# Kernel optimization log

Hardware: AMD Instinct MI355X
Metric: run time of the kernel (lower is better)

The kernel has to match this reference:

```python
import jax, jax.numpy as jnp
import numpy as np

T, B, XD, H, F = 1024, 256, 64, 256, 256  # seq_len, batch, x_dim, dim_RNN, feature dims
ALPHAS = [0.001, 0.01, 0.1]


def _alphas_per_unit():
    a = np.sort(np.asarray(ALPHAS, dtype=np.float32))
    assign = np.array([a[i % len(a)] for i in range(H)], dtype=np.float32)
    return jnp.asarray(np.sort(assign))  # [H]


def setup_inputs() -> dict:
    key = jax.random.key(0)
    ks = jax.random.split(key, 16)

    def w(k, shape, fan_in):
        return jax.random.normal(k, shape, jnp.float32) / np.sqrt(fan_in).astype(np.float32)

    return {
        "x": jax.random.normal(ks[0], (T, B, XD), jnp.float32),
        # feature_extractor_x: Linear(XD->F), Linear(F->F), tanh after each
        "Wx0": w(ks[1], (F, XD), XD), "bx0": jnp.zeros((F,), jnp.float32),
        "Wx1": w(ks[2], (F, F), F),   "bx1": jnp.zeros((F,), jnp.float32),
        # nn.RNN(F, H): tanh cell
        "Wih": w(ks[3], (H, F), F), "Whh": w(ks[4], (H, H), H),
        "bih": jnp.zeros((H,), jnp.float32), "bhh": jnp.zeros((H,), jnp.float32),
        # mlp_h_x: Linear(H->F), Linear(F->F), tanh after each
        "Wh0": w(ks[5], (F, H), H), "bh0": jnp.zeros((F,), jnp.float32),
        "Wh1": w(ks[6], (F, F), F), "bh1": jnp.zeros((F,), jnp.float32),
        # gen_out: Linear(F->XD)
        "Wg": w(ks[7], (XD, F), F), "bg": jnp.zeros((XD,), jnp.float32),
    }


def reference(x, Wx0, bx0, Wx1, bx1, Wih, Whh, bih, bhh, Wh0, bh0, Wh1, bh1, Wg, bg):
    act = jnp.tanh
    alphas = _alphas_per_unit()  # [H]

    # feature extractor applied to all timesteps at once (non-autonomous path)
    feat = act(jnp.einsum('tbx,fx->tbf', x, Wx0) + bx0)
    feat = act(jnp.einsum('tbf,gf->tbg', feat, Wx1) + bx1)  # [T,B,F]

    def step(h, ft):
        # y_t is generated from h BEFORE the recurrence update
        d = act(h @ Wh0.T + bh0)
        d = act(d @ Wh1.T + bh1)
        y = d @ Wg.T + bg  # [B,XD]
        h_raw = jnp.tanh(ft @ Wih.T + bih + h @ Whh.T + bhh)
        h_new = (1.0 - alphas) * h + alphas * h_raw  # leaky alpha-blend
        return h_new, y

    h0 = jnp.zeros((B, H), x.dtype)
    _, y = jax.lax.scan(step, h0, feat)  # y: [T,B,XD]
    return y
```

## Files before the change

### kernel.cpp

```cpp
#include <hip/hip_runtime.h>
#include <cstddef>


typedef _Float16 halfx8 __attribute__((ext_vector_type(8)));
typedef _Float16 halfx4 __attribute__((ext_vector_type(4)));
typedef float    f32x4  __attribute__((ext_vector_type(4)));

#define T_LEN 1024
#define B_SZ  256
#define H_DIM 256
#define M_ROWS (T_LEN * B_SZ)
#define MT     (M_ROWS / 32)
#define NRB    16
#define NGB    240

__device__ _Float16 gWx0[256 * 64];
__device__ _Float16 gWx1[256 * 256];
__device__ _Float16 gWih[256 * 256];
__device__ _Float16 gWh0[256 * 256];
__device__ _Float16 gWh1[256 * 256];
__device__ _Float16 gWg[64 * 256];
__device__ float gBx0[256], gBx1[256], gBih[256], gBh0[256], gBh1[256], gBg[64];
__device__ unsigned gProg[NRB];

__device__ __forceinline__ float fast_tanh(float x) {
  float e = __expf(2.0f * x);
  return 1.0f - 2.0f / (e + 1.0f);
}

__device__ __forceinline__ float alpha_of(int j) {
  return (j < 86) ? 0.001f : ((j < 171) ? 0.01f : 0.1f);
}

__device__ __forceinline__ void lds_barrier() {
  asm volatile("s_waitcnt lgkmcnt(0)\n\ts_barrier" ::: "memory");
}

__global__ void prep(const float* __restrict__ Wx0, const float* __restrict__ Wx1,
                     const float* __restrict__ Wih, const float* __restrict__ Wh0,
                     const float* __restrict__ Wh1, const float* __restrict__ Wg,
                     const float* __restrict__ bx0, const float* __restrict__ bx1,
                     const float* __restrict__ bih, const float* __restrict__ bh0,
                     const float* __restrict__ bh1, const float* __restrict__ bg) {
  const int i = blockIdx.x * blockDim.x + threadIdx.x;
  if (i < NRB) gProg[i] = 0u;
  if (i < 16384) { gWx0[i] = (_Float16)Wx0[i]; gWg[i] = (_Float16)Wg[i]; }
  if (i < 65536) {
    gWx1[i] = (_Float16)Wx1[i];
    gWih[i] = (_Float16)Wih[i];
    gWh0[i] = (_Float16)Wh0[i];
    gWh1[i] = (_Float16)Wh1[i];
  }
  if (i < 256) {
    gBx0[i] = bx0[i]; gBx1[i] = bx1[i]; gBih[i] = bih[i];
    gBh0[i] = bh0[i]; gBh1[i] = bh1[i];
  }
  if (i < 64) gBg[i] = bg[i];
}

template <int KCH, bool TANH>
__device__ __forceinline__ void stage_tile(const _Float16 (*__restrict__ Ah)[264],
                                           _Float16 (*__restrict__ Ch)[264],
                                           const _Float16* __restrict__ W,
                                           const float* __restrict__ bias,
                                           const int tid) {
  constexpr int K = KCH * 32;
  const int lane = tid & 63, wave = tid >> 6, l15 = lane & 15, quad = lane >> 4;
  const int jw = wave * 32;

  halfx8 Bf[2][KCH];
  float bcol[2];
  int jj[2];
#pragma unroll
  for (int nt = 0; nt < 2; nt++) {
    jj[nt] = jw + nt * 16 + l15;
    bcol[nt] = bias[jj[nt]];
#pragma unroll
    for (int ks = 0; ks < KCH; ks++)
      Bf[nt][ks] = *(const halfx8*)(W + (size_t)jj[nt] * K + ks * 32 + quad * 8);
  }

  f32x4 acc[2][2];
#pragma unroll
  for (int mi = 0; mi < 2; mi++)
#pragma unroll
    for (int nt = 0; nt < 2; nt++) acc[mi][nt] = (f32x4){0.f, 0.f, 0.f, 0.f};

#pragma unroll
  for (int ks = 0; ks < KCH; ks++)
#pragma unroll
    for (int mi = 0; mi < 2; mi++) {
      halfx8 a = *(const halfx8*)&Ah[mi * 16 + l15][ks * 32 + quad * 8];
#pragma unroll
      for (int nt = 0; nt < 2; nt++)
        acc[mi][nt] = __builtin_amdgcn_mfma_f32_16x16x32_f16(a, Bf[nt][ks], acc[mi][nt], 0, 0, 0);
    }

#pragma unroll
  for (int mi = 0; mi < 2; mi++)
#pragma unroll
    for (int nt = 0; nt < 2; nt++)
#pragma unroll
      for (int rg = 0; rg < 4; rg++) {
        float v = acc[mi][nt][rg] + bcol[nt];
        if (TANH) v = fast_tanh(v);
        Ch[mi * 16 + quad * 4 + rg][jj[nt]] = (_Float16)v;
      }
}

__device__ __forceinline__ void stage_zx(const _Float16 (*__restrict__ Ah)[264],
                                         _Float16* __restrict__ C,
                                         const _Float16* __restrict__ W,
                                         const float* __restrict__ bias,
                                         const int tid) {
  constexpr int KCH = 8, K = 256;
  const int lane = tid & 63, wave = tid >> 6, l15 = lane & 15, quad = lane >> 4;
  const int jw = wave * 32;

  halfx8 Bf[2][KCH];
  float bcol[2];
  int jj[2];
#pragma unroll
  for (int nt = 0; nt < 2; nt++) {
    jj[nt] = jw + nt * 16 + l15;
    bcol[nt] = bias[jj[nt]];
#pragma unroll
    for (int ks = 0; ks < KCH; ks++)
      Bf[nt][ks] = *(const halfx8*)(W + (size_t)jj[nt] * K + ks * 32 + quad * 8);
  }

  f32x4 acc[2][2];
#pragma unroll
  for (int mi = 0; mi < 2; mi++)
#pragma unroll
    for (int nt = 0; nt < 2; nt++) acc[mi][nt] = (f32x4){0.f, 0.f, 0.f, 0.f};

#pragma unroll
  for (int ks = 0; ks < KCH; ks++)
#pragma unroll
    for (int mi = 0; mi < 2; mi++) {
      halfx8 a = *(const halfx8*)&Ah[mi * 16 + l15][ks * 32 + quad * 8];
#pragma unroll
      for (int nt = 0; nt < 2; nt++)
        acc[mi][nt] = __builtin_amdgcn_mfma_f32_16x16x32_f16(a, Bf[nt][ks], acc[mi][nt], 0, 0, 0);
    }

#pragma unroll
  for (int mi = 0; mi < 2; mi++)
#pragma unroll
    for (int nt = 0; nt < 2; nt++)
#pragma unroll
      for (int rg = 0; rg < 4; rg++) {
        const int row = mi * 16 + quad * 4 + rg;
        C[(size_t)row * 256 + jj[nt]] = (_Float16)(acc[mi][nt][rg] + bcol[nt]);
      }
}

__device__ __forceinline__ void stage_out(const _Float16 (*__restrict__ Ah)[264],
                                          float* __restrict__ C,
                                          const _Float16* __restrict__ W,
                                          const float* __restrict__ bias,
                                          const int tid) {
  const int lane = tid & 63, wave = tid >> 6, l15 = lane & 15, quad = lane >> 4;
  if (wave < 4) {
    const int jcol = wave * 16 + l15;
    halfx8 Bf[8];
#pragma unroll
    for (int ks = 0; ks < 8; ks++)
      Bf[ks] = *(const halfx8*)(W + (size_t)jcol * 256 + ks * 32 + quad * 8);
    const float bc = bias[jcol];
    f32x4 acc[2];
#pragma unroll
    for (int mi = 0; mi < 2; mi++) acc[mi] = (f32x4){0.f, 0.f, 0.f, 0.f};
#pragma unroll
    for (int ks = 0; ks < 8; ks++)
#pragma unroll
      for (int mi = 0; mi < 2; mi++) {
        halfx8 a = *(const halfx8*)&Ah[mi * 16 + l15][ks * 32 + quad * 8];
        acc[mi] = __builtin_amdgcn_mfma_f32_16x16x32_f16(a, Bf[ks], acc[mi], 0, 0, 0);
      }
#pragma unroll
    for (int mi = 0; mi < 2; mi++)
#pragma unroll
      for (int rg = 0; rg < 4; rg++)
        C[(size_t)(mi * 16 + quad * 4 + rg) * 64 + jcol] = acc[mi][rg] + bc;
  }
}

__global__ __launch_bounds__(512, 2)
void pre(const float* __restrict__ x, _Float16* __restrict__ zx) {
  __shared__ __attribute__((aligned(16))) _Float16 lds[2][32][264];
  const int tid = threadIdx.x;
  _Float16(*Ah)[264] = lds[0];
  _Float16(*Bh)[264] = lds[1];

  for (int bm = blockIdx.x; bm < MT; bm += gridDim.x) {
    {
      const int srow = tid >> 4, sk4 = tid & 15;
      float4 tv = *(const float4*)(x + (size_t)(bm * 32 + srow) * 64 + sk4 * 4);
      halfx4 h;
      h[0] = (_Float16)tv.x; h[1] = (_Float16)tv.y;
      h[2] = (_Float16)tv.z; h[3] = (_Float16)tv.w;
      *(halfx4*)&Ah[srow][sk4 * 4] = h;
    }
    lds_barrier();
    stage_tile<2, true>(Ah, Bh, gWx0, gBx0, tid);
    lds_barrier();
    stage_tile<8, true>(Bh, Ah, gWx1, gBx1, tid);
    lds_barrier();
    stage_zx(Ah, zx + (size_t)bm * 32 * 256, gWih, gBih, tid);
    lds_barrier();
  }
}

__device__ void rnn_block(const _Float16* __restrict__ zx,
                          _Float16* __restrict__ h_all,
                          const float* __restrict__ Whh,
                          const float* __restrict__ bhh_p,
                          _Float16 (*__restrict__ lds)[264],
                          const int bid) {
  _Float16(*hB)[16][264] = reinterpret_cast<_Float16(*)[16][264]>(&lds[0][0]);

  const int tid  = threadIdx.x;
  const int lane = tid & 63;
  const int wave = tid >> 6;
  const int l15  = lane & 15;
  const int quad = lane >> 4;
  const int r0   = bid * 16;
  const int jb   = wave * 32;

  halfx8 Af[2][8];
#pragma unroll
  for (int mt = 0; mt < 2; mt++) {
    const int j = jb + mt * 16 + l15;
#pragma unroll
    for (int ks = 0; ks < 8; ks++) {
      const float* wp = Whh + (size_t)j * H_DIM + ks * 32 + quad * 8;
      float4 w0 = *(const float4*)wp;
      float4 w1 = *(const float4*)(wp + 4);
      halfx8 f;
      f[0] = (_Float16)w0.x; f[1] = (_Float16)w0.y;
      f[2] = (_Float16)w0.z; f[3] = (_Float16)w0.w;
      f[4] = (_Float16)w1.x; f[5] = (_Float16)w1.y;
      f[6] = (_Float16)w1.z; f[7] = (_Float16)w1.w;
      Af[mt][ks] = f;
    }
  }

  float bj[2][4], aj[2][4], oma[2][4];
#pragma unroll
  for (int mt = 0; mt < 2; mt++)
#pragma unroll
    for (int rg = 0; rg < 4; rg++) {
      const int j = jb + mt * 16 + quad * 4 + rg;
      bj[mt][rg]  = bhh_p[j];
      aj[mt][rg]  = alpha_of(j);
      oma[mt][rg] = 1.0f - aj[mt][rg];
    }

  for (int i = tid; i < 16 * 264; i += 512) (&hB[0][0][0])[i] = (_Float16)0.0f;
  __syncthreads();

  const _Float16* rdp[2] = {&hB[0][l15][quad * 8], &hB[1][l15][quad * 8]};
  _Float16*       wrp[2] = {&hB[1][l15][jb + quad * 4], &hB[0][l15][jb + quad * 4]};

  constexpr int STRIDE = B_SZ * H_DIM;
  const _Float16* zp = zx    + (size_t)(r0 + l15) * H_DIM + jb + quad * 4;
  _Float16*       hp = h_all + (size_t)(r0 + l15) * H_DIM + jb + quad * 4;

  float  zc[2][4];
  halfx4 zA[2];
  {
#pragma unroll
    for (int mt = 0; mt < 2; mt++) {
      halfx4 z0 = *(const halfx4*)(zp + mt * 16);
      zA[mt]    = *(const halfx4*)(zp + mt * 16 + STRIDE);
#pragma unroll
      for (int rg = 0; rg < 4; rg++) zc[mt][rg] = (float)z0[rg];
    }
    zp += 2 * (size_t)STRIDE;
  }

  float  hreg[2][4];
  halfx4 hh4[2];
#pragma unroll
  for (int mt = 0; mt < 2; mt++)
#pragma unroll
    for (int rg = 0; rg < 4; rg++) { hreg[mt][rg] = 0.0f; hh4[mt][rg] = (_Float16)0.0f; }

  auto step = [&](int p, bool pub, unsigned pval) {
    halfx4 znew[2];
#pragma unroll
    for (int mt = 0; mt < 2; mt++) znew[mt] = *(const halfx4*)(zp + mt * 16);
    zp += STRIDE;

    const _Float16* rd = rdp[p];
    halfx8 hb[8];
#pragma unroll
    for (int ks = 0; ks < 8; ks++) hb[ks] = *(const halfx8*)(rd + ks * 32);

    f32x4 acc[2];
#pragma unroll
    for (int mt = 0; mt < 2; mt++) acc[mt] = (f32x4){0.f, 0.f, 0.f, 0.f};
#pragma unroll
    for (int ks = 0; ks < 8; ks++)
#pragma unroll
      for (int mt = 0; mt < 2; mt++)
        acc[mt] = __builtin_amdgcn_mfma_f32_16x16x32_f16(Af[mt][ks], hb[ks], acc[mt], 0, 0, 0);

    _Float16* wr = wrp[p];
#pragma unroll
    for (int mt = 0; mt < 2; mt++) {
      halfx4 hnew;
#pragma unroll
      for (int rg = 0; rg < 4; rg++) {
        float hr = fast_tanh(zc[mt][rg] + acc[mt][rg] + bj[mt][rg]);
        float hn = oma[mt][rg] * hreg[mt][rg] + aj[mt][rg] * hr;
        hreg[mt][rg] = hn;
        hnew[rg] = (_Float16)hn;
      }
      __builtin_nontemporal_store(
          __builtin_bit_cast(unsigned long long, hh4[mt]),
          (unsigned long long*)(hp + mt * 16));
      hh4[mt] = hnew;
      *(halfx4*)(wr + mt * 16) = hnew;
    }
    hp += STRIDE;

    if (pub) {
      asm volatile("s_waitcnt vmcnt(0) lgkmcnt(0)\n\ts_barrier" ::: "memory");
      if (tid == 0)
        __hip_atomic_store(&gProg[bid], pval, __ATOMIC_RELEASE,
                           __HIP_MEMORY_SCOPE_AGENT);
    } else {
      lds_barrier();
    }

#pragma unroll
    for (int mt = 0; mt < 2; mt++) {
#pragma unroll
      for (int rg = 0; rg < 4; rg++) zc[mt][rg] = (float)zA[mt][rg];
      zA[mt] = znew[mt];
    }
  };

  for (int it = 0; it < T_LEN / 2; ++it) {
    const int t0 = 2 * it;
    step(0, false, 0u);
    step(1, (it & 7) == 7, (unsigned)(t0 + 2));
  }
}

__global__ __launch_bounds__(512, 1)
void mega2(const _Float16* __restrict__ zx, _Float16* __restrict__ h_all,
           float* __restrict__ out, const float* __restrict__ Whh,
           const float* __restrict__ bhh_p) {
  __shared__ __attribute__((aligned(16))) _Float16 lds[2][32][264];
  const int tid = threadIdx.x;

  if (blockIdx.x < NRB) {
    rnn_block(zx, h_all, Whh, bhh_p, lds[0], blockIdx.x);
    return;
  }

  const int g = blockIdx.x - NRB;
  _Float16(*Ah)[264] = lds[0];
  _Float16(*Bh)[264] = lds[1];

  for (int bm = g; bm < MT; bm += NGB) {
    const int t = bm >> 3, b2 = bm & 7;
    const unsigned need = (unsigned)(t + 1);
    if (tid == 0) {
      while (__hip_atomic_load(&gProg[2 * b2], __ATOMIC_RELAXED,
                               __HIP_MEMORY_SCOPE_AGENT) < need ||
             __hip_atomic_load(&gProg[2 * b2 + 1], __ATOMIC_RELAXED,
                               __HIP_MEMORY_SCOPE_AGENT) < need)
        __builtin_amdgcn_s_sleep(16);
      unsigned v = __hip_atomic_load(&gProg[2 * b2], __ATOMIC_ACQUIRE,
                                     __HIP_MEMORY_SCOPE_AGENT);
      asm volatile("" ::"v"(v));
    }
    __syncthreads();
    {
      const int srow = tid >> 4, sk4 = tid & 15;
      const _Float16* hsrc = h_all + (size_t)bm * 32 * 256 + (size_t)srow * 256 + sk4 * 16;
      halfx8 t0 = *(const halfx8*)hsrc;
      halfx8 t1 = *(const halfx8*)(hsrc + 8);
      *(halfx8*)&Ah[srow][sk4 * 16] = t0;
      *(halfx8*)&Ah[srow][sk4 * 16 + 8] = t1;
    }
    lds_barrier();
    stage_tile<8, true>(Ah, Bh, gWh0, gBh0, tid);
    lds_barrier();
    stage_tile<8, true>(Bh, Ah, gWh1, gBh1, tid);
    lds_barrier();
    stage_out(Ah, out + (size_t)bm * 32 * 64, gWg, gBg, tid);
    lds_barrier();
  }
}

extern "C" void kernel_launch(void* const* d_in, const int* in_sizes, int n_in,
                              void* d_out, int out_size, void* d_ws, size_t ws_size,
                              hipStream_t stream) {
  const float* x   = (const float*)d_in[0];
  const float* Wx0 = (const float*)d_in[1];
  const float* bx0 = (const float*)d_in[2];
  const float* Wx1 = (const float*)d_in[3];
  const float* bx1 = (const float*)d_in[4];
  const float* Wih = (const float*)d_in[5];
  const float* Whh = (const float*)d_in[6];
  const float* bih = (const float*)d_in[7];
  const float* bhh = (const float*)d_in[8];
  const float* Wh0 = (const float*)d_in[9];
  const float* bh0 = (const float*)d_in[10];
  const float* Wh1 = (const float*)d_in[11];
  const float* bh1 = (const float*)d_in[12];
  const float* Wg  = (const float*)d_in[13];
  const float* bg  = (const float*)d_in[14];
  float* out = (float*)d_out;

  _Float16* bufA = (_Float16*)d_ws;
  _Float16* bufB = bufA + (size_t)M_ROWS * 256;

  prep<<<256, 256, 0, stream>>>(Wx0, Wx1, Wih, Wh0, Wh1, Wg,
                                bx0, bx1, bih, bh0, bh1, bg);
  pre<<<512, 512, 0, stream>>>(x, bufA);
  mega2<<<NRB + NGB, 512, 0, stream>>>(bufA, bufB, out, Whh, bhh);
}
```

Measured before the change: 1.548 ms.

## Split fused feature-extractor kernel into three separate GEMM launches

Replaces the single fused pre kernel, which chained three GEMM stages through LDS, with three launches of a generic gemm8 kernel. The new kernel converts fp32 weights to fp16 itself, so prep no longer does that. Each stage now writes its fp16 intermediate to global memory and reads it back, adding memory traffic and launch overhead, while each kernel keeps a simpler register footprint. The change also halves how often the recurrent blocks publish progress (every 16 iterations instead of 8) and enlarges the mega2 LDS allocation, which looks unused and may reduce occupancy.

```diff
diff --git a/kernel.cpp b/kernel.cpp
--- a/kernel.cpp
+++ b/kernel.cpp
@@ -14,13 +14,10 @@
 #define NRB    16
 #define NGB    240
 
-__device__ _Float16 gWx0[256 * 64];
-__device__ _Float16 gWx1[256 * 256];
-__device__ _Float16 gWih[256 * 256];
 __device__ _Float16 gWh0[256 * 256];
 __device__ _Float16 gWh1[256 * 256];
 __device__ _Float16 gWg[64 * 256];
-__device__ float gBx0[256], gBx1[256], gBih[256], gBh0[256], gBh1[256], gBg[64];
+__device__ float gBh0[256], gBh1[256], gBg[64];
 __device__ unsigned gProg[NRB];
 
 __device__ __forceinline__ float fast_tanh(float x) {
@@ -36,26 +33,117 @@
   asm volatile("s_waitcnt lgkmcnt(0)\n\ts_barrier" ::: "memory");
 }
 
-__global__ void prep(const float* __restrict__ Wx0, const float* __restrict__ Wx1,
-                     const float* __restrict__ Wih, const float* __restrict__ Wh0,
-                     const float* __restrict__ Wh1, const float* __restrict__ Wg,
-                     const float* __restrict__ bx0, const float* __restrict__ bx1,
-                     const float* __restrict__ bih, const float* __restrict__ bh0,
+__global__ void prep(const float* __restrict__ Wh0, const float* __restrict__ Wh1,
+                     const float* __restrict__ Wg,  const float* __restrict__ bh0,
                      const float* __restrict__ bh1, const float* __restrict__ bg) {
   const int i = blockIdx.x * blockDim.x + threadIdx.x;
   if (i < NRB) gProg[i] = 0u;
-  if (i < 16384) { gWx0[i] = (_Float16)Wx0[i]; gWg[i] = (_Float16)Wg[i]; }
+  if (i < 16384) gWg[i] = (_Float16)Wg[i];
   if (i < 65536) {
-    gWx1[i] = (_Float16)Wx1[i];
-    gWih[i] = (_Float16)Wih[i];
     gWh0[i] = (_Float16)Wh0[i];
     gWh1[i] = (_Float16)Wh1[i];
   }
-  if (i < 256) {
-    gBx0[i] = bx0[i]; gBx1[i] = bx1[i]; gBih[i] = bih[i];
-    gBh0[i] = bh0[i]; gBh1[i] = bh1[i];
-  }
+  if (i < 256) { gBh0[i] = bh0[i]; gBh1[i] = bh1[i]; }
   if (i < 64) gBg[i] = bg[i];
+}
+
+template <int KCH, bool TANH, bool INF32>
+__global__ __launch_bounds__(512, 2)
+void gemm8(const void* __restrict__ Ap, const float* __restrict__ W,
+           const float* __restrict__ bias, void* __restrict__ Cp, int mtiles) {
+  constexpr int K  = KCH * 32;
+  constexpr int KP = K + 8;
+  __shared__ __attribute__((aligned(16))) _Float16 Ah[32][KP];
+
+  const int tid  = threadIdx.x;
+  const int lane = tid & 63;
+  const int wave = tid >> 6;
+  const int l15  = lane & 15;
+  const int quad = lane >> 4;
+  const int jw   = wave * 32;
+
+  halfx8 Bf[2][KCH];
+  float  bcol[2];
+  int    jj[2];
+#pragma unroll
+  for (int nt = 0; nt < 2; nt++) {
+    jj[nt]   = jw + nt * 16 + l15;
+    bcol[nt] = bias[jj[nt]];
+#pragma unroll
+    for (int ks = 0; ks < KCH; ks++) {
+      const float* wp = W + (size_t)jj[nt] * K + ks * 32 + quad * 8;
+      float4 w0 = *(const float4*)wp;
+      float4 w1 = *(const float4*)(wp + 4);
+      halfx8 f;
+      f[0] = (_Float16)w0.x; f[1] = (_Float16)w0.y;
+      f[2] = (_Float16)w0.z; f[3] = (_Float16)w0.w;
+      f[4] = (_Float16)w1.x; f[5] = (_Float16)w1.y;
+      f[6] = (_Float16)w1.z; f[7] = (_Float16)w1.w;
+      Bf[nt][ks] = f;
+    }
+  }
+
+  const int srow = tid >> 4;
+  const int sk4  = tid & 15;
+
+  for (int bm = blockIdx.x; bm < mtiles; bm += gridDim.x) {
+    if constexpr (INF32) {
+      const float* A = (const float*)Ap + (size_t)bm * 32 * K;
+      constexpr int SEG = K / 64;
+      float4 tv[SEG];
+#pragma unroll
+      for (int s = 0; s < SEG; s++)
+        tv[s] = *(const float4*)(A + (size_t)srow * K + (sk4 + s * 16) * 4);
+#pragma unroll
+      for (int s = 0; s < SEG; s++) {
+        halfx4 h;
+        h[0] = (_Float16)tv[s].x; h[1] = (_Float16)tv[s].y;
+        h[2] = (_Float16)tv[s].z; h[3] = (_Float16)tv[s].w;
+        *(halfx4*)&Ah[srow][(sk4 + s * 16) * 4] = h;
+      }
+    } else {
+      const _Float16* A = (const _Float16*)Ap + (size_t)bm * 32 * K;
+      constexpr int SEG = K / 128;
+      halfx8 tv[SEG];
+#pragma unroll
+      for (int s = 0; s < SEG; s++)
+        tv[s] = *(const halfx8*)(A + (size_t)srow * K + (sk4 + s * 16) * 8);
+#pragma unroll
+      for (int s = 0; s < SEG; s++)
+        *(halfx8*)&Ah[srow][(sk4 + s * 16) * 8] = tv[s];
+    }
+    lds_barrier();
+
+    f32x4 acc[2][2];
+#pragma unroll
+    for (int mi = 0; mi < 2; mi++)
+#pragma unroll
+      for (int nt = 0; nt < 2; nt++) acc[mi][nt] = (f32x4){0.f, 0.f, 0.f, 0.f};
+
+#pragma unroll
+    for (int ks = 0; ks < KCH; ks++)
+#pragma unroll
+      for (int mi = 0; mi < 2; mi++) {
+        halfx8 a = *(const halfx8*)&Ah[mi * 16 + l15][ks * 32 + quad * 8];
+#pragma unroll
+        for (int nt = 0; nt < 2; nt++)
+          acc[mi][nt] = __builtin_amdgcn_mfma_f32_16x16x32_f16(a, Bf[nt][ks], acc[mi][nt], 0, 0, 0);
+      }
+
+    _Float16* C = (_Float16*)Cp;
+#pragma unroll
+    for (int mi = 0; mi < 2; mi++)
+#pragma unroll
+      for (int nt = 0; nt < 2; nt++)
+#pragma unroll
+        for (int rg = 0; rg < 4; rg++) {
+          const int rowg = bm * 32 + mi * 16 + quad * 4 + rg;
+          float v = acc[mi][nt][rg] + bcol[nt];
+          if (TANH) v = fast_tanh(v);
+          C[(size_t)rowg * 256 + jj[nt]] = (_Float16)v;
+        }
+    lds_barrier();
+  }
 }
 
 template <int KCH, bool TANH>
@@ -108,54 +196,6 @@
       }
 }
 
-__device__ __forceinline__ void stage_zx(const _Float16 (*__restrict__ Ah)[264],
-                                         _Float16* __restrict__ C,
-                                         const _Float16* __restrict__ W,
-                                         const float* __restrict__ bias,
-                                         const int tid) {
-  constexpr int KCH = 8, K = 256;
-  const int lane = tid & 63, wave = tid >> 6, l15 = lane & 15, quad = lane >> 4;
-  const int jw = wave * 32;
-
-  halfx8 Bf[2][KCH];
-  float bcol[2];
-  int jj[2];
-#pragma unroll
-  for (int nt = 0; nt < 2; nt++) {
-    jj[nt] = jw + nt * 16 + l15;
-    bcol[nt] = bias[jj[nt]];
-#pragma unroll
-    for (int ks = 0; ks < KCH; ks++)
-      Bf[nt][ks] = *(const halfx8*)(W + (size_t)jj[nt] * K + ks * 32 + quad * 8);
-  }
-
-  f32x4 acc[2][2];
-#pragma unroll
-  for (int mi = 0; mi < 2; mi++)
-#pragma unroll
-    for (int nt = 0; nt < 2; nt++) acc[mi][nt] = (f32x4){0.f, 0.f, 0.f, 0.f};
-
-#pragma unroll
-  for (int ks = 0; ks < KCH; ks++)
-#pragma unroll
-    for (int mi = 0; mi < 2; mi++) {
-      halfx8 a = *(const halfx8*)&Ah[mi * 16 + l15][ks * 32 + quad * 8];
-#pragma unroll
-      for (int nt = 0; nt < 2; nt++)
-        acc[mi][nt] = __builtin_amdgcn_mfma_f32_16x16x32_f16(a, Bf[nt][ks], acc[mi][nt], 0, 0, 0);
-    }
-
-#pragma unroll
-  for (int mi = 0; mi < 2; mi++)
-#pragma unroll
-    for (int nt = 0; nt < 2; nt++)
-#pragma unroll
-      for (int rg = 0; rg < 4; rg++) {
-        const int row = mi * 16 + quad * 4 + rg;
-        C[(size_t)row * 256 + jj[nt]] = (_Float16)(acc[mi][nt][rg] + bcol[nt]);
-      }
-}
-
 __device__ __forceinline__ void stage_out(const _Float16 (*__restrict__ Ah)[264],
                                           float* __restrict__ C,
                                           const _Float16* __restrict__ W,
@@ -184,32 +224,6 @@
 #pragma unroll
       for (int rg = 0; rg < 4; rg++)
         C[(size_t)(mi * 16 + quad * 4 + rg) * 64 + jcol] = acc[mi][rg] + bc;
-  }
-}
-
-__global__ __launch_bounds__(512, 2)
-void pre(const float* __restrict__ x, _Float16* __restrict__ zx) {
-  __shared__ __attribute__((aligned(16))) _Float16 lds[2][32][264];
-  const int tid = threadIdx.x;
-  _Float16(*Ah)[264] = lds[0];
-  _Float16(*Bh)[264] = lds[1];
-
-  for (int bm = blockIdx.x; bm < MT; bm += gridDim.x) {
-    {
-      const int srow = tid >> 4, sk4 = tid & 15;
-      float4 tv = *(const float4*)(x + (size_t)(bm * 32 + srow) * 64 + sk4 * 4);
-      halfx4 h;
-      h[0] = (_Float16)tv.x; h[1] = (_Float16)tv.y;
-      h[2] = (_Float16)tv.z; h[3] = (_Float16)tv.w;
-      *(halfx4*)&Ah[srow][sk4 * 4] = h;
-    }
-    lds_barrier();
-    stage_tile<2, true>(Ah, Bh, gWx0, gBx0, tid);
-    lds_barrier();
-    stage_tile<8, true>(Bh, Ah, gWx1, gBx1, tid);
-    lds_barrier();
-    stage_zx(Ah, zx + (size_t)bm * 32 * 256, gWih, gBih, tid);
-    lds_barrier();
   }
 }
 
@@ -347,7 +361,7 @@
   for (int it = 0; it < T_LEN / 2; ++it) {
     const int t0 = 2 * it;
     step(0, false, 0u);
-    step(1, (it & 7) == 7, (unsigned)(t0 + 2));
+    step(1, (it & 15) == 15, (unsigned)(t0 + 2));
   }
 }
 
@@ -355,7 +369,7 @@
 void mega2(const _Float16* __restrict__ zx, _Float16* __restrict__ h_all,
            float* __restrict__ out, const float* __restrict__ Whh,
            const float* __restrict__ bhh_p) {
-  __shared__ __attribute__((aligned(16))) _Float16 lds[2][32][264];
+  __shared__ __attribute__((aligned(16))) _Float16 lds[5][32][264];
   const int tid = threadIdx.x;
 
   if (blockIdx.x < NRB) {
@@ -422,8 +436,9 @@
   _Float16* bufA = (_Float16*)d_ws;
   _Float16* bufB = bufA + (size_t)M_ROWS * 256;
 
-  prep<<<256, 256, 0, stream>>>(Wx0, Wx1, Wih, Wh0, Wh1, Wg,
-                                bx0, bx1, bih, bh0, bh1, bg);
-  pre<<<512, 512, 0, stream>>>(x, bufA);
+  prep<<<256, 256, 0, stream>>>(Wh0, Wh1, Wg, bh0, bh1, bg);
+  gemm8<2, true, true><<<512, 512, 0, stream>>>(x, Wx0, bx0, bufA, MT);
+  gemm8<8, true, false><<<512, 512, 0, stream>>>(bufA, Wx1, bx1, bufB, MT);
+  gemm8<8, false, false><<<512, 512, 0, stream>>>(bufB, Wih, bih, bufA, MT);
   mega2<<<NRB + NGB, 512, 0, stream>>>(bufA, bufB, out, Whh, bhh);
 }
```

After: 1.411 ms. 1.1x faster.
